# Kernel optimization log

Hardware: AMD Instinct MI355X
Metric: run time of the kernel (lower is better)

The kernel has to match this reference:

```python
import jax, jax.numpy as jnp
import numpy as np

B, S, D, H = 4, 2048, 1024, 16
HD = D // H
EPS = 1e-5


def gelu_tanh(x):
    c = jnp.sqrt(jnp.asarray(2.0 / jnp.pi, x.dtype))
    return x * 0.5 * (1.0 + jnp.tanh(c * (x + 0.044715 * x ** 3)))


def layer_norm(x, scale, shift):
    mean = jnp.mean(x, axis=-1, keepdims=True)
    var = jnp.var(x, axis=-1, keepdims=True)  # unbiased=False
    return scale * ((x - mean) / jnp.sqrt(var + EPS)) + shift


def setup_inputs() -> dict:
    key = jax.random.key(0)
    ks = jax.random.split(key, 8)
    s = 0.02
    return {
        "x": jax.random.normal(ks[0], (B, S, D), jnp.float32),
        "Wqkv": jax.random.normal(ks[1], (D, 3 * D), jnp.float32) * s,
        "Wout": jax.random.normal(ks[2], (D, D), jnp.float32) * s,
        "bout": jnp.zeros((D,), jnp.float32),
        "W1": jax.random.normal(ks[3], (D, 4 * D), jnp.float32) * s,
        "b1": jnp.zeros((4 * D,), jnp.float32),
        "W2": jax.random.normal(ks[4], (4 * D, D), jnp.float32) * s,
        "b2": jnp.zeros((D,), jnp.float32),
        "g1": jnp.ones((D,), jnp.float32),
        "s1": jnp.zeros((D,), jnp.float32),
        "g2": jnp.ones((D,), jnp.float32),
        "s2": jnp.zeros((D,), jnp.float32),
    }


def reference(x, Wqkv, Wout, bout, W1, b1, W2, b2, g1, s1, g2, s2):
    # --- attention branch ---
    h = layer_norm(x, g1, s1)
    qkv = h @ Wqkv  # [B,S,3D]
    qkv = qkv.reshape(B, S, 3, H, HD).transpose(2, 0, 3, 1, 4)  # [3,B,H,S,hd]
    q, k, v = qkv[0], qkv[1], qkv[2]
    scores = jnp.einsum("bhqd,bhkd->bhqk", q, k)
    causal = jnp.triu(jnp.ones((S, S), bool), k=1)
    scores = jnp.where(causal, -jnp.inf, scores)
    attn = jax.nn.softmax(scores / jnp.sqrt(jnp.asarray(HD, x.dtype)), axis=-1)
    ctx = jnp.einsum("bhqk,bhkd->bhqd", attn, v)
    ctx = ctx.transpose(0, 2, 1, 3).reshape(B, S, D)
    x = x + (ctx @ Wout + bout)
    # --- MLP branch ---
    h = layer_norm(x, g2, s2)
    h = gelu_tanh(h @ W1 + b1) @ W2 + b2
    return x + h
```

## Files before the change

### kernel.cpp

```cpp
#include <hip/hip_runtime.h>
#include <stdint.h>

typedef unsigned short u16;
typedef unsigned long long u64;
typedef __attribute__((ext_vector_type(8))) short bf16x8;
typedef __attribute__((ext_vector_type(4))) float f32x4;

#define DEV __device__ __forceinline__

DEV u16 f2bf(float f) {
  union { float f; unsigned u; } v; v.f = f;
  unsigned r = (v.u + 0x7fffu + ((v.u >> 16) & 1u)) >> 16;
  return (u16)r;
}

#define GLDS(g, l) __builtin_amdgcn_global_load_lds( \
    (const __attribute__((address_space(1))) void*)(g), \
    (__attribute__((address_space(3))) void*)(l), 16, 0, 0)

__global__ __launch_bounds__(256) void k_transpose_all(
    const float* __restrict__ Wqkv, const float* __restrict__ Wout,
    const float* __restrict__ W1, const float* __restrict__ W2,
    u16* __restrict__ WqkvT, u16* __restrict__ WoutT,
    u16* __restrict__ W1T, u16* __restrict__ W2T) {
  int id = blockIdx.x;
  const float* in; u16* out; int K, N, nx, base;
  if (id < 3072)      { in = Wqkv; out = WqkvT; K = 1024; N = 3072; nx = 96;  base = 0; }
  else if (id < 4096) { in = Wout; out = WoutT; K = 1024; N = 1024; nx = 32;  base = 3072; }
  else if (id < 8192) { in = W1;   out = W1T;   K = 1024; N = 4096; nx = 128; base = 4096; }
  else                { in = W2;   out = W2T;   K = 4096; N = 1024; nx = 32;  base = 8192; }
  int seg = id - base, bx = seg % nx, by = seg / nx;
  __shared__ float tile[32][33];
  int tx = threadIdx.x & 31, ty = threadIdx.x >> 5;
#pragma unroll
  for (int r = 0; r < 32; r += 8)
    tile[ty + r][tx] = in[(size_t)(by * 32 + ty + r) * N + bx * 32 + tx];
  __syncthreads();
#pragma unroll
  for (int r = 0; r < 32; r += 8)
    out[(size_t)(bx * 32 + ty + r) * K + by * 32 + tx] = f2bf(tile[tx][ty + r]);
}

__global__ __launch_bounds__(256) void k_layernorm(
    const float* __restrict__ x, const float* __restrict__ gamma,
    const float* __restrict__ beta, u16* __restrict__ out) {
  int row = blockIdx.x, t = threadIdx.x;
  const float4 v = ((const float4*)(x + (size_t)row * 1024))[t];
  float sum = v.x + v.y + v.z + v.w;
  float sq = v.x * v.x + v.y * v.y + v.z * v.z + v.w * v.w;
#pragma unroll
  for (int o = 32; o >= 1; o >>= 1) {
    sum += __shfl_down(sum, o);
    sq += __shfl_down(sq, o);
  }
  __shared__ float red[8];
  if ((t & 63) == 0) { red[(t >> 6) * 2] = sum; red[(t >> 6) * 2 + 1] = sq; }
  __syncthreads();
  sum = red[0] + red[2] + red[4] + red[6];
  sq = red[1] + red[3] + red[5] + red[7];
  float mean = sum * (1.0f / 1024.0f);
  float var = sq * (1.0f / 1024.0f) - mean * mean;
  float rstd = rsqrtf(var + 1e-5f);
  float4 g = ((const float4*)gamma)[t];
  float4 b = ((const float4*)beta)[t];
  ushort4 o4;
  o4.x = f2bf(g.x * (v.x - mean) * rstd + b.x);
  o4.y = f2bf(g.y * (v.y - mean) * rstd + b.y);
  o4.z = f2bf(g.z * (v.z - mean) * rstd + b.z);
  o4.w = f2bf(g.w * (v.w - mean) * rstd + b.w);
  ((ushort4*)(out + (size_t)row * 1024))[t] = o4;
}

struct EpiQKV {
  u16 *Q, *K2, *VT;
  DEV void operator()(int r, int c0, const f32x4& v) const {
    int three = c0 >> 10, h = (c0 >> 6) & 15, hd = c0 & 63;
    int b = r >> 11, s = r & 2047;
    int bh = b * 16 + h;
    ushort4 o;
    o.x = f2bf(v[0]); o.y = f2bf(v[1]); o.z = f2bf(v[2]); o.w = f2bf(v[3]);
    if (three == 0)
      *(ushort4*)&Q[((size_t)bh * 2048 + s) * 64 + hd] = o;
    else if (three == 1)
      *(ushort4*)&K2[((size_t)bh * 2048 + s) * 64 + hd] = o;
    else {
      VT[((size_t)bh * 64 + hd + 0) * 2048 + s] = o.x;
      VT[((size_t)bh * 64 + hd + 1) * 2048 + s] = o.y;
      VT[((size_t)bh * 64 + hd + 2) * 2048 + s] = o.z;
      VT[((size_t)bh * 64 + hd + 3) * 2048 + s] = o.w;
    }
  }
};

struct EpiBiasResid {
  const float* bias; const float* resid; float* out; int N;
  DEV void operator()(int r, int c0, const f32x4& v) const {
    size_t idx = (size_t)r * N + c0;
    float4 bb = *(const float4*)&bias[c0];
    float4 rr = *(const float4*)&resid[idx];
    float4 o;
    o.x = v[0] + bb.x + rr.x; o.y = v[1] + bb.y + rr.y;
    o.z = v[2] + bb.z + rr.z; o.w = v[3] + bb.w + rr.w;
    *(float4*)&out[idx] = o;
  }
};

struct EpiBiasGelu {
  const float* bias; u16* out; int N;
  DEV float gelu(float xx) const {
    float u = 0.7978845608f * (xx + 0.044715f * xx * xx * xx);
    float e = __expf(2.0f * u);
    float th = 1.0f - 2.0f / (e + 1.0f);
    return 0.5f * xx * (1.0f + th);
  }
  DEV void operator()(int r, int c0, const f32x4& v) const {
    float4 bb = *(const float4*)&bias[c0];
    ushort4 o;
    o.x = f2bf(gelu(v[0] + bb.x)); o.y = f2bf(gelu(v[1] + bb.y));
    o.z = f2bf(gelu(v[2] + bb.z)); o.w = f2bf(gelu(v[3] + bb.w));
    *(ushort4*)&out[(size_t)r * N + c0] = o;
  }
};

template <typename Epi>
__global__ __launch_bounds__(256) void k_gemm_tn(
    const u16* __restrict__ A, const u16* __restrict__ Bt, int K, Epi epi) {
  __shared__ u16 As[2][128 * 32];
  __shared__ u16 Bs[2][128 * 32];
  const int t = threadIdx.x;
  const int bm = blockIdx.x, bn = blockIdx.y;
  const int lane = t & 63, w = t >> 6;
  const int wm = w >> 1, wn = w & 1;
  const int quad = lane >> 4, l16 = lane & 15;
  f32x4 acc[4][4] = {};
  const u16* gA = A + (size_t)(bm * 128 + (t >> 2)) * K + (t & 3) * 8;
  const u16* gB = Bt + (size_t)(bn * 128 + (t >> 2)) * K + (t & 3) * 8;
  u16* lA0 = &As[0][t * 8]; u16* lA1 = &As[1][t * 8];
  u16* lB0 = &Bs[0][t * 8]; u16* lB1 = &Bs[1][t * 8];
  for (int k0 = 0; k0 < K; k0 += 64) {
    __syncthreads();
    GLDS(gA, lA0);      GLDS(gA + (size_t)64 * K, lA0 + 2048);
    GLDS(gA + 32, lA1); GLDS(gA + 32 + (size_t)64 * K, lA1 + 2048);
    GLDS(gB, lB0);      GLDS(gB + (size_t)64 * K, lB0 + 2048);
    GLDS(gB + 32, lB1); GLDS(gB + 32 + (size_t)64 * K, lB1 + 2048);
    gA += 64; gB += 64;
    __syncthreads();
#pragma unroll
    for (int kk = 0; kk < 2; ++kk) {
      bf16x8 af[4], bfr[4];
#pragma unroll
      for (int mt = 0; mt < 4; ++mt)
        af[mt] = *(const bf16x8*)&As[kk][(wm * 64 + mt * 16 + l16) * 32 + quad * 8];
#pragma unroll
      for (int nt = 0; nt < 4; ++nt)
        bfr[nt] = *(const bf16x8*)&Bs[kk][(wn * 64 + nt * 16 + l16) * 32 + quad * 8];
#pragma unroll
      for (int mt = 0; mt < 4; ++mt)
#pragma unroll
        for (int nt = 0; nt < 4; ++nt)
          acc[mt][nt] = __builtin_amdgcn_mfma_f32_16x16x32_bf16(
              bfr[nt], af[mt], acc[mt][nt], 0, 0, 0);
    }
  }
  const int r0 = bm * 128 + wm * 64 + l16;
  const int c0 = bn * 128 + wn * 64 + quad * 4;
#pragma unroll
  for (int mt = 0; mt < 4; ++mt)
#pragma unroll
    for (int nt = 0; nt < 4; ++nt)
      epi(r0 + mt * 16, c0 + nt * 16, acc[mt][nt]);
}

#define PW 72

__global__ __launch_bounds__(256) void k_attn(
    const u16* __restrict__ Qg, const u16* __restrict__ Kg,
    const u16* __restrict__ VTg, u16* __restrict__ ctx) {
  const int bh = blockIdx.x;
  const int qt = 31 - blockIdx.y;
  const int b = bh >> 4, h = bh & 15;
  const int t = threadIdx.x, lane = t & 63, w = t >> 6;
  const int quad = lane >> 4, l16 = lane & 15;
  const int q0 = qt * 64;
  __shared__ u16 Qs[64 * PW], Ks[64 * PW], Vs[64 * PW];
  __shared__ u16 Ps[4][16 * PW];
  __shared__ float l_lds[4][16];
  const u16* Qbase = Qg + (size_t)bh * (2048 * 64);
  const u16* Kbase = Kg + (size_t)bh * (2048 * 64);
  const u16* Vbase = VTg + (size_t)bh * (64 * 2048);
#pragma unroll
  for (int j = 0; j < 4; ++j) {
    int ch = t + 256 * j, r = ch >> 4, cc = (ch & 15) * 4;
    *(u64*)&Qs[r * PW + cc] = *(const u64*)(Qbase + (size_t)(q0 + r) * 64 + cc);
  }
  __syncthreads();
  bf16x8 qf0 = *(const bf16x8*)&Qs[(w * 16 + l16) * PW + quad * 8];
  bf16x8 qf1 = *(const bf16x8*)&Qs[(w * 16 + l16) * PW + 32 + quad * 8];
  const int qrow = q0 + w * 16 + l16;
  const float c1 = 0.18033688011f;
  float lsum = 0.f;
  f32x4 acco[4] = {};
  for (int kt = 0; kt <= qt; ++kt) {
    const int k0 = kt * 64;
    __syncthreads();
#pragma unroll
    for (int j = 0; j < 4; ++j) {
      int ch = t + 256 * j, r = ch >> 4, cc = (ch & 15) * 4;
      *(u64*)&Ks[r * PW + cc] =
          *(const u64*)(Kbase + (size_t)(k0 + r) * 64 + cc);
      *(u64*)&Vs[r * PW + cc] =
          *(const u64*)(Vbase + (size_t)r * 2048 + k0 + cc);
    }
    __syncthreads();
    f32x4 sacc[4] = {};
#pragma unroll
    for (int kk = 0; kk < 2; ++kk) {
      bf16x8 qf = kk ? qf1 : qf0;
#pragma unroll
      for (int nt = 0; nt < 4; ++nt) {
        bf16x8 kf = *(const bf16x8*)&Ks[(nt * 16 + l16) * PW + kk * 32 + quad * 8];
        sacc[nt] = __builtin_amdgcn_mfma_f32_16x16x32_bf16(kf, qf, sacc[nt], 0, 0, 0);
      }
    }
    const bool diag = (kt == qt);
    float ls = 0.f;
#pragma unroll
    for (int nt = 0; nt < 4; ++nt) {
      ushort4 o;
#pragma unroll
      for (int reg = 0; reg < 4; ++reg) {
        float p = __builtin_amdgcn_exp2f(sacc[nt][reg] * c1);
        if (diag && (k0 + nt * 16 + quad * 4 + reg > qrow)) p = 0.f;
        ls += p;
        (&o.x)[reg] = f2bf(p);
      }
      *(ushort4*)&Ps[w][l16 * PW + nt * 16 + quad * 4] = o;
    }
    ls += __shfl_xor(ls, 16);
    ls += __shfl_xor(ls, 32);
    lsum += ls;
#pragma unroll
    for (int kk = 0; kk < 2; ++kk) {
      bf16x8 pf = *(const bf16x8*)&Ps[w][l16 * PW + kk * 32 + quad * 8];
#pragma unroll
      for (int nt = 0; nt < 4; ++nt) {
        bf16x8 vf = *(const bf16x8*)&Vs[(nt * 16 + l16) * PW + kk * 32 + quad * 8];
        acco[nt] = __builtin_amdgcn_mfma_f32_16x16x32_bf16(pf, vf, acco[nt], 0, 0, 0);
      }
    }
  }
  if (quad == 0) l_lds[w][l16] = lsum;
  float4 lv = *(const float4*)&l_lds[w][quad * 4];
  float inv[4];
  inv[0] = 1.0f / lv.x; inv[1] = 1.0f / lv.y;
  inv[2] = 1.0f / lv.z; inv[3] = 1.0f / lv.w;
#pragma unroll
  for (int nt = 0; nt < 4; ++nt)
#pragma unroll
    for (int reg = 0; reg < 4; ++reg) {
      float o = acco[nt][reg] * inv[reg];
      int q = q0 + w * 16 + quad * 4 + reg;
      ctx[((size_t)(b * 2048 + q)) * 1024 + h * 64 + nt * 16 + l16] = f2bf(o);
    }
}

extern "C" void kernel_launch(void* const* d_in, const int* in_sizes, int n_in,
                              void* d_out, int out_size, void* d_ws, size_t ws_size,
                              hipStream_t stream) {
  (void)in_sizes; (void)n_in; (void)out_size; (void)ws_size;
  const float* x    = (const float*)d_in[0];
  const float* Wqkv = (const float*)d_in[1];
  const float* Wout = (const float*)d_in[2];
  const float* bout = (const float*)d_in[3];
  const float* W1   = (const float*)d_in[4];
  const float* b1   = (const float*)d_in[5];
  const float* W2   = (const float*)d_in[6];
  const float* b2   = (const float*)d_in[7];
  const float* g1   = (const float*)d_in[8];
  const float* s1   = (const float*)d_in[9];
  const float* g2   = (const float*)d_in[10];
  const float* s2   = (const float*)d_in[11];

  char* ws = (char*)d_ws;
  u16*   WqkvT = (u16*)(ws + 0);
  u16*   WoutT = (u16*)(ws + 6291456);
  u16*   W1T   = (u16*)(ws + 8388608);
  u16*   W2T   = (u16*)(ws + 16777216);
  float* x1    = (float*)(ws + 25165824);
  u16*   h12   = (u16*)(ws + 58720256);
  u16*   Qb    = (u16*)(ws + 75497472);
  u16*   Kb    = (u16*)(ws + 92274688);
  u16*   VTb   = (u16*)(ws + 109051904);
  u16*   ctx   = (u16*)(ws + 125829120);
  u16*   a1    = (u16*)(ws + 75497472);

  k_transpose_all<<<12288, 256, 0, stream>>>(Wqkv, Wout, W1, W2,
                                             WqkvT, WoutT, W1T, W2T);

  k_layernorm<<<8192, 256, 0, stream>>>(x, g1, s1, h12);
  k_gemm_tn<<<dim3(64, 24), 256, 0, stream>>>(h12, WqkvT, 1024,
                                              EpiQKV{Qb, Kb, VTb});
  k_attn<<<dim3(64, 32), 256, 0, stream>>>(Qb, Kb, VTb, ctx);
  k_gemm_tn<<<dim3(64, 8), 256, 0, stream>>>(ctx, WoutT, 1024,
                                             EpiBiasResid{bout, x, x1, 1024});
  k_layernorm<<<8192, 256, 0, stream>>>(x1, g2, s2, h12);
  k_gemm_tn<<<dim3(64, 32), 256, 0, stream>>>(h12, W1T, 1024,
                                              EpiBiasGelu{b1, a1, 4096});
  k_gemm_tn<<<dim3(64, 8), 256, 0, stream>>>(a1, W2T, 4096,
                                             EpiBiasResid{b2, x1, (float*)d_out, 1024});
}
```

Before: 556.8 us.

## Replace GEMM with 256x256-tile, 512-thread pipelined kernel with swizzled LDS

Replaces the 128x128 double-buffered GEMM with a 256x256 tile kernel using 8 waves, a K-step of 64, an XOR-swizzled LDS layout and a hand-scheduled pipeline. Global-to-LDS loads for the next tiles are interleaved with MFMA groups using explicit barriers, waitcnts and setprio. Workgroup ids are remapped across XCDs. The aim is more data reuse per tile, fewer LDS bank conflicts and better overlap of loads with matrix math. The cost is large LDS use (128KB) and register pressure. The smaller N=1024 GEMMs launch only 128 workgroups, which may leave CUs idle.

```diff
diff --git a/kernel.cpp b/kernel.cpp
--- a/kernel.cpp
+++ b/kernel.cpp
@@ -17,6 +17,10 @@
 #define GLDS(g, l) __builtin_amdgcn_global_load_lds( \
     (const __attribute__((address_space(1))) void*)(g), \
     (__attribute__((address_space(3))) void*)(l), 16, 0, 0)
+
+#define BAR() __builtin_amdgcn_s_barrier()
+#define LGKM0() asm volatile("s_waitcnt lgkmcnt(0)" ::: "memory")
+#define VMW(n) asm volatile("s_waitcnt vmcnt(" #n ")" ::: "memory")
 
 __global__ __launch_bounds__(256) void k_transpose_all(
     const float* __restrict__ Wqkv, const float* __restrict__ Wout,
@@ -122,50 +126,111 @@
   }
 };
 
+#define STAGE_A(tk, d, h) do { \
+  GLDS(gA + (size_t)((h) * 128) * K + (tk) * 64, \
+       &As[(d)][((h) * 128) * 64 + t * 8]); \
+  GLDS(gA + (size_t)((h) * 128 + 64) * K + (tk) * 64, \
+       &As[(d)][((h) * 128 + 64) * 64 + t * 8]); \
+} while (0)
+#define STAGE_B(tk, d, h) do { \
+  GLDS(gB + (size_t)((h) * 128) * K + (tk) * 64, \
+       &Bs[(d)][((h) * 128) * 64 + t * 8]); \
+  GLDS(gB + (size_t)((h) * 128 + 64) * K + (tk) * 64, \
+       &Bs[(d)][((h) * 128 + 64) * 64 + t * 8]); \
+} while (0)
+
+#define LDAQ(d_, mh) \
+  _Pragma("unroll") for (int mt = 0; mt < 4; ++mt) \
+  _Pragma("unroll") for (int kk = 0; kk < 2; ++kk) \
+    af[mt][kk] = *(const bf16x8*)((const char*)&As[(d_)][0] + \
+        ((wm * 128 + (mh) * 64 + mt * 16 + l16) * 128 + \
+         ((kk * 64 + quad * 16) ^ swz)))
+
+#define LDBQ(d_, nh) \
+  _Pragma("unroll") for (int nt = 0; nt < 2; ++nt) \
+  _Pragma("unroll") for (int kk = 0; kk < 2; ++kk) \
+    bf[(nh) * 2 + nt][kk] = *(const bf16x8*)((const char*)&Bs[(d_)][0] + \
+        ((wn * 64 + ((nh) * 2 + nt) * 16 + l16) * 128 + \
+         ((kk * 64 + quad * 16) ^ swz)))
+
+#define MM(mh, nh) do { \
+  __builtin_amdgcn_s_setprio(1); \
+  _Pragma("unroll") for (int mt = 0; mt < 4; ++mt) \
+  _Pragma("unroll") for (int nt = 0; nt < 2; ++nt) \
+  _Pragma("unroll") for (int kk = 0; kk < 2; ++kk) \
+    acc[(mh) * 4 + mt][(nh) * 2 + nt] = \
+        __builtin_amdgcn_mfma_f32_16x16x32_bf16( \
+            bf[(nh) * 2 + nt][kk], af[mt][kk], \
+            acc[(mh) * 4 + mt][(nh) * 2 + nt], 0, 0, 0); \
+  __builtin_amdgcn_s_setprio(0); \
+} while (0)
+
+#define GROUP(T_, d_) do { \
+  const int Tg = (T_); const int dg = (d_); \
+  const bool stA = Tg + 1 < NT, stB = Tg + 2 < NT; \
+  LDAQ(dg, 0); \
+  LDBQ(dg, 0); \
+  if (stA) STAGE_A(Tg + 1, (dg) ^ 1, 0); \
+  BAR(); LGKM0(); \
+  MM(0, 0); \
+  BAR(); \
+  LDBQ(dg, 1); \
+  if (stA) STAGE_A(Tg + 1, (dg) ^ 1, 1); \
+  BAR(); LGKM0(); \
+  MM(0, 1); \
+  BAR(); \
+  LDAQ(dg, 1); \
+  if (stB) STAGE_B(Tg + 2, dg, 0); \
+  BAR(); LGKM0(); \
+  MM(1, 1); \
+  BAR(); \
+  if (stB) STAGE_B(Tg + 2, dg, 1); \
+  BAR(); \
+  MM(1, 0); \
+  if (stB) { VMW(4); } else { VMW(0); } \
+  BAR(); \
+} while (0)
+
 template <typename Epi>
-__global__ __launch_bounds__(256) void k_gemm_tn(
+__global__ __launch_bounds__(512, 2) void k_gemm256(
     const u16* __restrict__ A, const u16* __restrict__ Bt, int K, Epi epi) {
-  __shared__ u16 As[2][128 * 32];
-  __shared__ u16 Bs[2][128 * 32];
+  __shared__ __align__(16) u16 As[2][256 * 64];
+  __shared__ __align__(16) u16 Bs[2][256 * 64];
   const int t = threadIdx.x;
-  const int bm = blockIdx.x, bn = blockIdx.y;
+  int id = blockIdx.x;
+  {
+    int nwg = gridDim.x;
+    if (!(nwg & 7)) id = (id & 7) * (nwg >> 3) + (id >> 3);
+  }
+  const int bm = id & 31, bn = id >> 5;
   const int lane = t & 63, w = t >> 6;
-  const int wm = w >> 1, wn = w & 1;
+  const int wm = w >> 2, wn = w & 3;
   const int quad = lane >> 4, l16 = lane & 15;
-  f32x4 acc[4][4] = {};
-  const u16* gA = A + (size_t)(bm * 128 + (t >> 2)) * K + (t & 3) * 8;
-  const u16* gB = Bt + (size_t)(bn * 128 + (t >> 2)) * K + (t & 3) * 8;
-  u16* lA0 = &As[0][t * 8]; u16* lA1 = &As[1][t * 8];
-  u16* lB0 = &Bs[0][t * 8]; u16* lB1 = &Bs[1][t * 8];
-  for (int k0 = 0; k0 < K; k0 += 64) {
-    __syncthreads();
-    GLDS(gA, lA0);      GLDS(gA + (size_t)64 * K, lA0 + 2048);
-    GLDS(gA + 32, lA1); GLDS(gA + 32 + (size_t)64 * K, lA1 + 2048);
-    GLDS(gB, lB0);      GLDS(gB + (size_t)64 * K, lB0 + 2048);
-    GLDS(gB + 32, lB1); GLDS(gB + 32 + (size_t)64 * K, lB1 + 2048);
-    gA += 64; gB += 64;
-    __syncthreads();
-#pragma unroll
-    for (int kk = 0; kk < 2; ++kk) {
-      bf16x8 af[4], bfr[4];
-#pragma unroll
-      for (int mt = 0; mt < 4; ++mt)
-        af[mt] = *(const bf16x8*)&As[kk][(wm * 64 + mt * 16 + l16) * 32 + quad * 8];
-#pragma unroll
-      for (int nt = 0; nt < 4; ++nt)
-        bfr[nt] = *(const bf16x8*)&Bs[kk][(wn * 64 + nt * 16 + l16) * 32 + quad * 8];
-#pragma unroll
-      for (int mt = 0; mt < 4; ++mt)
-#pragma unroll
-        for (int nt = 0; nt < 4; ++nt)
-          acc[mt][nt] = __builtin_amdgcn_mfma_f32_16x16x32_bf16(
-              bfr[nt], af[mt], acc[mt][nt], 0, 0, 0);
-    }
-  }
-  const int r0 = bm * 128 + wm * 64 + l16;
-  const int c0 = bn * 128 + wn * 64 + quad * 4;
-#pragma unroll
-  for (int mt = 0; mt < 4; ++mt)
+  const int swz = (l16 & 7) << 4;
+  const int NT = K >> 6;
+  const int srow = t >> 3, sslot = (t & 7) ^ (srow & 7);
+  const u16* gA = A + (size_t)(bm * 256 + srow) * K + sslot * 8;
+  const u16* gB = Bt + (size_t)(bn * 256 + srow) * K + sslot * 8;
+
+  f32x4 acc[8][4] = {};
+  bf16x8 af[4][2], bf[4][2];
+
+  STAGE_B(0, 0, 0); STAGE_B(0, 0, 1);
+  STAGE_A(0, 0, 0); STAGE_A(0, 0, 1);
+  STAGE_B(1, 1, 0); STAGE_B(1, 1, 1);
+  VMW(4);
+  BAR();
+
+#pragma unroll 1
+  for (int T = 0; T < NT; T += 2) {
+    GROUP(T, 0);
+    GROUP(T + 1, 1);
+  }
+
+  const int r0 = bm * 256 + wm * 128 + l16;
+  const int c0 = bn * 256 + wn * 64 + quad * 4;
+#pragma unroll
+  for (int mt = 0; mt < 8; ++mt)
 #pragma unroll
     for (int nt = 0; nt < 4; ++nt)
       epi(r0 + mt * 16, c0 + nt * 16, acc[mt][nt]);
@@ -298,14 +363,12 @@
                                              WqkvT, WoutT, W1T, W2T);
 
   k_layernorm<<<8192, 256, 0, stream>>>(x, g1, s1, h12);
-  k_gemm_tn<<<dim3(64, 24), 256, 0, stream>>>(h12, WqkvT, 1024,
-                                              EpiQKV{Qb, Kb, VTb});
+  k_gemm256<<<384, 512, 0, stream>>>(h12, WqkvT, 1024, EpiQKV{Qb, Kb, VTb});
   k_attn<<<dim3(64, 32), 256, 0, stream>>>(Qb, Kb, VTb, ctx);
-  k_gemm_tn<<<dim3(64, 8), 256, 0, stream>>>(ctx, WoutT, 1024,
-                                             EpiBiasResid{bout, x, x1, 1024});
+  k_gemm256<<<128, 512, 0, stream>>>(ctx, WoutT, 1024,
+                                     EpiBiasResid{bout, x, x1, 1024});
   k_layernorm<<<8192, 256, 0, stream>>>(x1, g2, s2, h12);
-  k_gemm_tn<<<dim3(64, 32), 256, 0, stream>>>(h12, W1T, 1024,
-                                              EpiBiasGelu{b1, a1, 4096});
-  k_gemm_tn<<<dim3(64, 8), 256, 0, stream>>>(a1, W2T, 4096,
-                                             EpiBiasResid{b2, x1, (float*)d_out, 1024});
-}
+  k_gemm256<<<512, 512, 0, stream>>>(h12, W1T, 1024, EpiBiasGelu{b1, a1, 4096});
+  k_gemm256<<<128, 512, 0, stream>>>(a1, W2T, 4096,
+                                     EpiBiasResid{b2, x1, (float*)d_out, 1024});
+}
```

After: 578.2 us. 3.8% more time.

## Double-buffer GEMM LDS tiles with async global_load_lds prefetch two stages ahead

Applied to the files above, without the earlier changes.

Adds a second LDS buffer stage to the bf16 GEMM so the global-to-LDS loads for tile T+2 are issued while tile T+1 is still in flight. Partial vmcnt waits and raw s_barrier replace the load-then-sync pattern, which stalled every iteration on memory. LDS use doubles to 64KB per block, which may lower occupancy, and the waitcnt and barrier ordering has to be exactly right to avoid reading partly loaded tiles.

```diff
diff --git a/kernel.cpp b/kernel.cpp
--- a/kernel.cpp
+++ b/kernel.cpp
@@ -17,6 +17,10 @@
 #define GLDS(g, l) __builtin_amdgcn_global_load_lds( \
     (const __attribute__((address_space(1))) void*)(g), \
     (__attribute__((address_space(3))) void*)(l), 16, 0, 0)
+
+#define BAR() __builtin_amdgcn_s_barrier()
+#define VMW(n) asm volatile("s_waitcnt vmcnt(" #n ")" ::: "memory")
+#define SCHED0() __builtin_amdgcn_sched_barrier(0)
 
 __global__ __launch_bounds__(256) void k_transpose_all(
     const float* __restrict__ Wqkv, const float* __restrict__ Wout,
@@ -122,11 +126,22 @@
   }
 };
 
+#define STG8(tk, d) do { \
+    GLDS(gA + (tk) * 64,                        &As[d][0][t * 8]); \
+    GLDS(gA + (tk) * 64 + (size_t)64 * K,       &As[d][0][t * 8 + 2048]); \
+    GLDS(gA + (tk) * 64 + 32,                   &As[d][1][t * 8]); \
+    GLDS(gA + (tk) * 64 + 32 + (size_t)64 * K,  &As[d][1][t * 8 + 2048]); \
+    GLDS(gB + (tk) * 64,                        &Bs[d][0][t * 8]); \
+    GLDS(gB + (tk) * 64 + (size_t)64 * K,       &Bs[d][0][t * 8 + 2048]); \
+    GLDS(gB + (tk) * 64 + 32,                   &Bs[d][1][t * 8]); \
+    GLDS(gB + (tk) * 64 + 32 + (size_t)64 * K,  &Bs[d][1][t * 8 + 2048]); \
+  } while (0)
+
 template <typename Epi>
 __global__ __launch_bounds__(256) void k_gemm_tn(
     const u16* __restrict__ A, const u16* __restrict__ Bt, int K, Epi epi) {
-  __shared__ u16 As[2][128 * 32];
-  __shared__ u16 Bs[2][128 * 32];
+  __shared__ u16 As[2][2][128 * 32];
+  __shared__ u16 Bs[2][2][128 * 32];
   const int t = threadIdx.x;
   const int bm = blockIdx.x, bn = blockIdx.y;
   const int lane = t & 63, w = t >> 6;
@@ -135,25 +150,24 @@
   f32x4 acc[4][4] = {};
   const u16* gA = A + (size_t)(bm * 128 + (t >> 2)) * K + (t & 3) * 8;
   const u16* gB = Bt + (size_t)(bn * 128 + (t >> 2)) * K + (t & 3) * 8;
-  u16* lA0 = &As[0][t * 8]; u16* lA1 = &As[1][t * 8];
-  u16* lB0 = &Bs[0][t * 8]; u16* lB1 = &Bs[1][t * 8];
-  for (int k0 = 0; k0 < K; k0 += 64) {
-    __syncthreads();
-    GLDS(gA, lA0);      GLDS(gA + (size_t)64 * K, lA0 + 2048);
-    GLDS(gA + 32, lA1); GLDS(gA + 32 + (size_t)64 * K, lA1 + 2048);
-    GLDS(gB, lB0);      GLDS(gB + (size_t)64 * K, lB0 + 2048);
-    GLDS(gB + 32, lB1); GLDS(gB + 32 + (size_t)64 * K, lB1 + 2048);
-    gA += 64; gB += 64;
-    __syncthreads();
+  const int NT = K >> 6;
+
+  STG8(0, 0);
+  STG8(1, 1);
+  VMW(8);
+  BAR();
+
+  for (int T = 0; T < NT; ++T) {
+    const int d = T & 1;
 #pragma unroll
     for (int kk = 0; kk < 2; ++kk) {
       bf16x8 af[4], bfr[4];
 #pragma unroll
       for (int mt = 0; mt < 4; ++mt)
-        af[mt] = *(const bf16x8*)&As[kk][(wm * 64 + mt * 16 + l16) * 32 + quad * 8];
+        af[mt] = *(const bf16x8*)&As[d][kk][(wm * 64 + mt * 16 + l16) * 32 + quad * 8];
 #pragma unroll
       for (int nt = 0; nt < 4; ++nt)
-        bfr[nt] = *(const bf16x8*)&Bs[kk][(wn * 64 + nt * 16 + l16) * 32 + quad * 8];
+        bfr[nt] = *(const bf16x8*)&Bs[d][kk][(wn * 64 + nt * 16 + l16) * 32 + quad * 8];
 #pragma unroll
       for (int mt = 0; mt < 4; ++mt)
 #pragma unroll
@@ -161,7 +175,18 @@
           acc[mt][nt] = __builtin_amdgcn_mfma_f32_16x16x32_bf16(
               bfr[nt], af[mt], acc[mt][nt], 0, 0, 0);
     }
-  }
+    SCHED0();
+    BAR();
+    SCHED0();
+    if (T + 2 < NT) {
+      STG8(T + 2, d);
+      VMW(8);
+    } else {
+      VMW(0);
+    }
+    BAR();
+  }
+
   const int r0 = bm * 128 + wm * 64 + l16;
   const int c0 = bn * 128 + wn * 64 + quad * 4;
 #pragma unroll
```

Measured after the change: 535.8 us. 3.8% less time.
